# Optimization experiments

Measured on AMD Instinct MI355X. Metric: run time of the kernel, lower is better.

## Reference

```python
import jax, jax.numpy as jnp
import numpy as np

B, N, A, D = 1, 10000, 32, 256
H, DH = 4, 64


def setup_inputs() -> dict:
    key = jax.random.key(0)
    ks = jax.random.split(key, 9)
    x = jax.random.normal(ks[0], (B, N, D), dtype=jnp.float32)
    adj_kv_indices = jax.random.randint(ks[1], (B, N, A), 0, N, dtype=jnp.int64)
    mask = jax.random.randint(ks[2], (B, N, A), 0, 2) > 0
    Wq = jax.random.normal(ks[3], (D, H * DH), dtype=jnp.float32) * 0.02
    Wkv = jax.random.normal(ks[4], (D, 2 * H * DH), dtype=jnp.float32) * 0.02
    Wo = jax.random.normal(ks[5], (H * DH, D), dtype=jnp.float32) * 0.02
    bo = jnp.zeros((D,), dtype=jnp.float32)
    null_k = jax.random.normal(ks[6], (H, DH), dtype=jnp.float32)
    null_v = jax.random.normal(ks[7], (H, DH), dtype=jnp.float32)
    return {"x": x, "adj_kv_indices": adj_kv_indices, "mask": mask,
            "Wq": Wq, "Wkv": Wkv, "Wo": Wo, "bo": bo,
            "null_k": null_k, "null_v": null_v}


def reference(x, adj_kv_indices, mask, Wq, Wkv, Wo, bo, null_k, null_v):
    b, n, d = x.shape
    a = adj_kv_indices.shape[-1]
    h, dh = null_k.shape
    scale = dh ** -0.5

    # gather neighbor features: [b, n, a, d]
    kv_x = jnp.take_along_axis(x, adj_kv_indices.reshape(b, n * a)[:, :, None], axis=1)
    kv_x = kv_x.reshape(b, n, a, d)

    q = (x @ Wq).reshape(b, n, h, dh).transpose(0, 2, 1, 3)          # b h n dh
    kv = kv_x @ Wkv                                                   # b n a 2*h*dh
    k, v = jnp.split(kv, 2, axis=-1)
    k = k.reshape(b, n, a, h, dh).transpose(0, 3, 1, 2, 4)            # b h n a dh
    v = v.reshape(b, n, a, h, dh).transpose(0, 3, 1, 2, 4)

    # prepend null key/value token
    nk = jnp.broadcast_to(null_k[None, :, None, None, :], (b, h, n, 1, dh))
    nv = jnp.broadcast_to(null_v[None, :, None, None, :], (b, h, n, 1, dh))
    k = jnp.concatenate([nk, k], axis=-2)                             # b h n (a+1) dh
    v = jnp.concatenate([nv, v], axis=-2)

    full_mask = jnp.pad(mask, ((0, 0), (0, 0), (1, 0)), constant_values=True)
    full_mask = full_mask[:, None, :, :]                              # b 1 n (a+1)

    sim = jnp.einsum('bhnd,bhnad->bhna', q, k) * scale
    mask_value = -jnp.finfo(sim.dtype).max
    sim = jnp.where(full_mask, sim, mask_value)
    attn = jax.nn.softmax(sim, axis=-1)
    out = jnp.einsum('bhna,bhnad->bhnd', attn, v)
    out = out.transpose(0, 2, 1, 3).reshape(b, n, h * dh)
    return out @ Wo + bo
```

## Files before the change

kernel.cpp:

```cpp
#include <hip/hip_runtime.h>
#include <float.h>


typedef _Float16 f16;
typedef _Float16 f16x4 __attribute__((ext_vector_type(4)));
typedef _Float16 f16x8 __attribute__((ext_vector_type(8)));
typedef float    f32x4 __attribute__((ext_vector_type(4)));

#define BM 64
#define BN 128
#define BK 64
#define LDK 72

__global__ __launch_bounds__(256) void tcast_kernel(
    const float* __restrict__ W, f16* __restrict__ Wt, int K, int Nn, float mul)
{
    __shared__ float s[32][33];
    const int tx = threadIdx.x & 31, ty = threadIdx.x >> 5;
    const int kb = blockIdx.y * 32, nb = blockIdx.x * 32;
#pragma unroll
    for (int r = 0; r < 4; r++)
        s[ty + r * 8][tx] = W[(size_t)(kb + ty + r * 8) * Nn + nb + tx];
    __syncthreads();
#pragma unroll
    for (int r = 0; r < 4; r++)
        Wt[(size_t)(nb + ty + r * 8) * K + kb + tx] = (f16)(s[tx][ty + r * 8] * mul);
}

template <int A_F32, int OUT_HALF>
__global__ __launch_bounds__(256) void hgemm_kernel(
    const void* __restrict__ Av, const f16* __restrict__ Bt,
    void* __restrict__ C, const float* __restrict__ bias,
    int M, int Nn, int K)
{
    __shared__ f16 As[BM][LDK];
    __shared__ f16 Bs[BN][LDK];
    const int tid = threadIdx.x;
    const int w = tid >> 6;
    const int l = tid & 63;
    const int brow = blockIdx.y * BM;
    const int bcol = blockIdx.x * BN;

    const int sra = tid >> 2, sca = (tid & 3) * 16;
    const int srb = tid >> 1, scb = (tid & 1) * 32;
    const int arow = min(brow + sra, M - 1);

    const int fr = l & 15;
    const int k4 = (l >> 4) * 4;

    f32x4 acc[8];
#pragma unroll
    for (int c = 0; c < 8; c++) acc[c] = (f32x4){0.f, 0.f, 0.f, 0.f};

    for (int kk = 0; kk < K; kk += BK) {
        if (A_F32) {
            const float* ap = (const float*)Av + (size_t)arow * K + kk + sca;
#pragma unroll
            for (int i = 0; i < 4; i++) {
                float4 v = ((const float4*)ap)[i];
                f16x4 o = {(f16)v.x, (f16)v.y, (f16)v.z, (f16)v.w};
                *(f16x4*)&As[sra][sca + i * 4] = o;
            }
        } else {
            const f16* ap = (const f16*)Av + (size_t)arow * K + kk + sca;
            *(f16x8*)&As[sra][sca]     = *(const f16x8*)(ap);
            *(f16x8*)&As[sra][sca + 8] = *(const f16x8*)(ap + 8);
        }
        {
            const f16* bp = Bt + (size_t)(bcol + srb) * K + kk + scb;
#pragma unroll
            for (int i = 0; i < 4; i++)
                *(f16x8*)&Bs[srb][scb + i * 8] = *(const f16x8*)(bp + i * 8);
        }
        __syncthreads();
#pragma unroll
        for (int k0 = 0; k0 < BK; k0 += 16) {
            f16x4 af = *(const f16x4*)&As[w * 16 + fr][k0 + k4];
#pragma unroll
            for (int c = 0; c < 8; c++) {
                f16x4 bf = *(const f16x4*)&Bs[c * 16 + fr][k0 + k4];
                acc[c] = __builtin_amdgcn_mfma_f32_16x16x16f16(af, bf, acc[c], 0, 0, 0);
            }
        }
        __syncthreads();
    }

#pragma unroll
    for (int c = 0; c < 8; c++) {
        const int col = bcol + c * 16 + fr;
#pragma unroll
        for (int j = 0; j < 4; j++) {
            const int row = brow + w * 16 + (l >> 4) * 4 + j;
            if (row < M) {
                if (OUT_HALF)
                    ((f16*)C)[(size_t)row * Nn + col] = (f16)acc[c][j];
                else
                    ((float*)C)[(size_t)row * Nn + col] = acc[c][j] + bias[col];
            }
        }
    }
}

__global__ __launch_bounds__(256) void attn_kernel(
    const f16* __restrict__ QKV,
    const int* __restrict__ aidx, const int* __restrict__ amask,
    const float* __restrict__ nullk, const float* __restrict__ nullv,
    f16* __restrict__ out)
{
    const int n    = blockIdx.x;
    const int tid  = threadIdx.x;
    const int w    = tid >> 6;
    const int h    = w;
    const int lane = tid & 63;
    const int g    = lane >> 4;
    const int gl   = lane & 15;

    __shared__ int   sIdx[32];
    __shared__ int   sMsk[32];
    __shared__ float sP[4][33];

    if (tid < 32) {
        sIdx[tid] = aidx[n * 32 + tid];
        sMsk[tid] = amask[n * 32 + tid];
    }
    __syncthreads();

    f16x4 qh = *(const f16x4*)(QKV + (size_t)n * 768 + h * 64 + gl * 4);
    const float q0 = (float)qh[0], q1 = (float)qh[1], q2 = (float)qh[2], q3 = (float)qh[3];

    float sim[9];

    {
        float s;
        if (g == 0) {
            float4 nk4 = ((const float4*)nullk)[h * 16 + gl];
            s = q0 * nk4.x + q1 * nk4.y + q2 * nk4.z + q3 * nk4.w;
        } else {
            int j = sIdx[g - 1];
            f16x4 kh = *(const f16x4*)(QKV + (size_t)j * 768 + 256 + h * 64 + gl * 4);
            s = q0 * (float)kh[0] + q1 * (float)kh[1] + q2 * (float)kh[2] + q3 * (float)kh[3];
        }
        s += __shfl_xor(s, 1); s += __shfl_xor(s, 2);
        s += __shfl_xor(s, 4); s += __shfl_xor(s, 8);
        bool ok = (g == 0) || (sMsk[g - 1] != 0);
        sim[0] = ok ? s : -3.0e38f;
    }

#pragma unroll
    for (int r = 1; r < 9; r++) {
        int a  = r * 4 + g;
        int ai = min(a - 1, 31);
        int j  = sIdx[ai];
        f16x4 kh = *(const f16x4*)(QKV + (size_t)j * 768 + 256 + h * 64 + gl * 4);
        float s = q0 * (float)kh[0] + q1 * (float)kh[1] + q2 * (float)kh[2] + q3 * (float)kh[3];
        s += __shfl_xor(s, 1); s += __shfl_xor(s, 2);
        s += __shfl_xor(s, 4); s += __shfl_xor(s, 8);
        bool ok = (a < 33) && (sMsk[ai] != 0);
        sim[r] = ok ? s : -3.0e38f;
    }

    float m = sim[0];
#pragma unroll
    for (int r = 1; r < 9; r++) m = fmaxf(m, sim[r]);
    m = fmaxf(m, __shfl_xor(m, 16));
    m = fmaxf(m, __shfl_xor(m, 32));

    float p[9]; float l = 0.0f;
#pragma unroll
    for (int r = 0; r < 9; r++) {
        p[r] = (sim[r] > -1.0e37f) ? __expf(sim[r] - m) : 0.0f;
        l += p[r];
    }
    l += __shfl_xor(l, 16);
    l += __shfl_xor(l, 32);
    const float inv = 1.0f / l;

    if (gl == 0) {
#pragma unroll
        for (int r = 0; r < 9; r++) {
            int a = r * 4 + g;
            if (a < 33) sP[w][a] = p[r] * inv;
        }
    }
    __syncthreads();

    float acc = sP[w][0] * nullv[h * 64 + lane];
#pragma unroll
    for (int a = 1; a <= 32; a++) {
        int j = sIdx[a - 1];
        float va = (float)QKV[(size_t)j * 768 + 512 + h * 64 + lane];
        acc += sP[w][a] * va;
    }
    out[(size_t)n * 256 + h * 64 + lane] = (f16)acc;
}

extern "C" void kernel_launch(void* const* d_in, const int* in_sizes, int n_in,
                              void* d_out, int out_size, void* d_ws, size_t ws_size,
                              hipStream_t stream)
{
    const float* x     = (const float*)d_in[0];
    const int*   aidx  = (const int*)  d_in[1];
    const int*   amask = (const int*)  d_in[2];
    const float* Wq    = (const float*)d_in[3];
    const float* Wkv   = (const float*)d_in[4];
    const float* Wo    = (const float*)d_in[5];
    const float* bo    = (const float*)d_in[6];
    const float* nk    = (const float*)d_in[7];
    const float* nv    = (const float*)d_in[8];
    float* out = (float*)d_out;

    const int N = 10000;
    f16* Wqkvt = (f16*)d_ws;
    f16* Wot   = Wqkvt + 768 * 256;
    f16* QKV   = Wot   + 256 * 256;
    f16* AOh   = QKV   + (size_t)N * 768;

    dim3 blk(256);
    tcast_kernel<<<dim3(8,  8), blk, 0, stream>>>(Wq,  Wqkvt,             256, 256, 0.125f);
    tcast_kernel<<<dim3(16, 8), blk, 0, stream>>>(Wkv, Wqkvt + 256 * 256, 256, 512, 1.0f);
    tcast_kernel<<<dim3(8,  8), blk, 0, stream>>>(Wo,  Wot,               256, 256, 1.0f);

    const int gm = (N + BM - 1) / BM;
    hgemm_kernel<1, 1><<<dim3(768 / BN, gm), blk, 0, stream>>>(x,   Wqkvt, QKV, nullptr, N, 768, 256);
    attn_kernel       <<<dim3(N),              blk, 0, stream>>>(QKV, aidx, amask, nk, nv, AOh);
    hgemm_kernel<0, 0><<<dim3(256 / BN, gm), blk, 0, stream>>>(AOh, Wot,   out, bo,      N, 256, 256);
}
```

Baseline: 150.2 us.

## Retile GEMM to 128x128 with direct global-to-LDS loads and 16x16x32 MFMA

The GEMM kernel now uses 128x128 tiles with a 2x2 wave layout. Each wave computes a 64x64 sub-tile as 4x4 MFMA accumulators using the wider 16x16x32 f16 instruction, and tiles are loaded with global_load_lds directly into unpadded LDS. The fp32 x input is no longer converted to f16 inside the GEMM; a separate cast kernel does it beforehand, which adds a launch and an extra round trip of x through memory. The aim is more register-level reuse and fewer LDS store instructions, at the cost of possible LDS bank conflicts from the unpadded layout and fewer blocks for the small output GEMM.

```diff
diff --git a/kernel.cpp b/kernel.cpp
--- a/kernel.cpp
+++ b/kernel.cpp
@@ -1,5 +1,4 @@
 #include <hip/hip_runtime.h>
-#include <float.h>
 
 
 typedef _Float16 f16;
@@ -7,10 +6,29 @@
 typedef _Float16 f16x8 __attribute__((ext_vector_type(8)));
 typedef float    f32x4 __attribute__((ext_vector_type(4)));
 
-#define BM 64
-#define BN 128
-#define BK 64
-#define LDK 72
+#define TM 128
+#define TN 128
+#define TK 32
+
+__device__ __forceinline__ void gload16(const f16* g, f16* l) {
+    __builtin_amdgcn_global_load_lds(
+        (const __attribute__((address_space(1))) unsigned int*)g,
+        (__attribute__((address_space(3))) unsigned int*)l,
+        16, 0, 0);
+}
+
+__global__ __launch_bounds__(256) void cast_kernel(
+    const float* __restrict__ in, f16* __restrict__ out, int n8)
+{
+    int i = blockIdx.x * 256 + threadIdx.x;
+    if (i < n8) {
+        float4 a = ((const float4*)in)[i * 2];
+        float4 b = ((const float4*)in)[i * 2 + 1];
+        f16x8 o = {(f16)a.x, (f16)a.y, (f16)a.z, (f16)a.w,
+                   (f16)b.x, (f16)b.y, (f16)b.z, (f16)b.w};
+        ((f16x8*)out)[i] = o;
+    }
+}
 
 __global__ __launch_bounds__(256) void tcast_kernel(
     const float* __restrict__ W, f16* __restrict__ Wt, int K, int Nn, float mul)
@@ -27,75 +45,69 @@
         Wt[(size_t)(nb + ty + r * 8) * K + kb + tx] = (f16)(s[tx][ty + r * 8] * mul);
 }
 
-template <int A_F32, int OUT_HALF>
+template <int OUT_F32>
 __global__ __launch_bounds__(256) void hgemm_kernel(
-    const void* __restrict__ Av, const f16* __restrict__ Bt,
+    const f16* __restrict__ A, const f16* __restrict__ Bt,
     void* __restrict__ C, const float* __restrict__ bias,
     int M, int Nn, int K)
 {
-    __shared__ f16 As[BM][LDK];
-    __shared__ f16 Bs[BN][LDK];
+    __shared__ f16 As[TM * TK];
+    __shared__ f16 Bs[TN * TK];
     const int tid = threadIdx.x;
-    const int w = tid >> 6;
-    const int l = tid & 63;
-    const int brow = blockIdx.y * BM;
-    const int bcol = blockIdx.x * BN;
-
-    const int sra = tid >> 2, sca = (tid & 3) * 16;
-    const int srb = tid >> 1, scb = (tid & 1) * 32;
-    const int arow = min(brow + sra, M - 1);
-
-    const int fr = l & 15;
-    const int k4 = (l >> 4) * 4;
-
-    f32x4 acc[8];
-#pragma unroll
-    for (int c = 0; c < 8; c++) acc[c] = (f32x4){0.f, 0.f, 0.f, 0.f};
-
-    for (int kk = 0; kk < K; kk += BK) {
-        if (A_F32) {
-            const float* ap = (const float*)Av + (size_t)arow * K + kk + sca;
-#pragma unroll
-            for (int i = 0; i < 4; i++) {
-                float4 v = ((const float4*)ap)[i];
-                f16x4 o = {(f16)v.x, (f16)v.y, (f16)v.z, (f16)v.w};
-                *(f16x4*)&As[sra][sca + i * 4] = o;
-            }
-        } else {
-            const f16* ap = (const f16*)Av + (size_t)arow * K + kk + sca;
-            *(f16x8*)&As[sra][sca]     = *(const f16x8*)(ap);
-            *(f16x8*)&As[sra][sca + 8] = *(const f16x8*)(ap + 8);
-        }
-        {
-            const f16* bp = Bt + (size_t)(bcol + srb) * K + kk + scb;
-#pragma unroll
-            for (int i = 0; i < 4; i++)
-                *(f16x8*)&Bs[srb][scb + i * 8] = *(const f16x8*)(bp + i * 8);
-        }
+    const int w  = tid >> 6, l = tid & 63;
+    const int fr = l & 15,  h = l >> 4;
+    const int brow = blockIdx.y * TM, bcol = blockIdx.x * TN;
+    const int wr = (w >> 1) * 64, wc = (w & 1) * 64;
+
+    const int c1 = tid, c2 = tid + 256;
+    const size_t aoff1 = (size_t)min(brow + (c1 >> 2), M - 1) * K + (c1 & 3) * 8;
+    const size_t aoff2 = (size_t)min(brow + (c2 >> 2), M - 1) * K + (c2 & 3) * 8;
+    const size_t boff1 = (size_t)(bcol + (c1 >> 2)) * K + (c1 & 3) * 8;
+    const size_t boff2 = (size_t)(bcol + (c2 >> 2)) * K + (c2 & 3) * 8;
+
+    f32x4 acc[4][4];
+#pragma unroll
+    for (int m = 0; m < 4; m++)
+#pragma unroll
+        for (int n = 0; n < 4; n++) acc[m][n] = (f32x4){0.f, 0.f, 0.f, 0.f};
+
+    for (int kk = 0; kk < K; kk += TK) {
+        gload16(A  + aoff1 + kk, &As[c1 * 8]);
+        gload16(A  + aoff2 + kk, &As[c2 * 8]);
+        gload16(Bt + boff1 + kk, &Bs[c1 * 8]);
+        gload16(Bt + boff2 + kk, &Bs[c2 * 8]);
         __syncthreads();
-#pragma unroll
-        for (int k0 = 0; k0 < BK; k0 += 16) {
-            f16x4 af = *(const f16x4*)&As[w * 16 + fr][k0 + k4];
-#pragma unroll
-            for (int c = 0; c < 8; c++) {
-                f16x4 bf = *(const f16x4*)&Bs[c * 16 + fr][k0 + k4];
-                acc[c] = __builtin_amdgcn_mfma_f32_16x16x16f16(af, bf, acc[c], 0, 0, 0);
-            }
-        }
+
+        f16x8 af[4], bf[4];
+#pragma unroll
+        for (int m = 0; m < 4; m++)
+            af[m] = *(const f16x8*)&As[(wr + m * 16 + fr) * TK + h * 8];
+#pragma unroll
+        for (int n = 0; n < 4; n++)
+            bf[n] = *(const f16x8*)&Bs[(wc + n * 16 + fr) * TK + h * 8];
+#pragma unroll
+        for (int m = 0; m < 4; m++)
+#pragma unroll
+            for (int n = 0; n < 4; n++)
+                acc[m][n] = __builtin_amdgcn_mfma_f32_16x16x32_f16(
+                    af[m], bf[n], acc[m][n], 0, 0, 0);
         __syncthreads();
     }
 
 #pragma unroll
-    for (int c = 0; c < 8; c++) {
-        const int col = bcol + c * 16 + fr;
-#pragma unroll
-        for (int j = 0; j < 4; j++) {
-            const int row = brow + w * 16 + (l >> 4) * 4 + j;
-            if (row < M) {
-                if (OUT_HALF)
-                    ((f16*)C)[(size_t)row * Nn + col] = (f16)acc[c][j];
-                else
-                    ((float*)C)[(size_t)row * Nn + col] = acc[c][j] + bias[col];
+    for (int m = 0; m < 4; m++) {
+#pragma unroll
+        for (int n = 0; n < 4; n++) {
+            const int col = bcol + wc + n * 16 + fr;
+#pragma unroll
+            for (int j = 0; j < 4; j++) {
+                const int row = brow + wr + m * 16 + h * 4 + j;
+                if (row < M) {
+                    if (OUT_F32)
+                        ((float*)C)[(size_t)row * Nn + col] = acc[m][n][j] + bias[col];
+                    else
+                        ((f16*)C)[(size_t)row * Nn + col] = (f16)acc[m][n][j];
+                }
             }
         }
     }
@@ -210,18 +222,20 @@
     float* out = (float*)d_out;
 
     const int N = 10000;
-    f16* Wqkvt = (f16*)d_ws;
+    f16* xh    = (f16*)d_ws;
+    f16* Wqkvt = xh    + (size_t)N * 256;
     f16* Wot   = Wqkvt + 768 * 256;
     f16* QKV   = Wot   + 256 * 256;
     f16* AOh   = QKV   + (size_t)N * 768;
 
     dim3 blk(256);
+    cast_kernel<<<dim3(N * 256 / 8 / 256 + 1), blk, 0, stream>>>(x, xh, N * 256 / 8);
     tcast_kernel<<<dim3(8,  8), blk, 0, stream>>>(Wq,  Wqkvt,             256, 256, 0.125f);
     tcast_kernel<<<dim3(16, 8), blk, 0, stream>>>(Wkv, Wqkvt + 256 * 256, 256, 512, 1.0f);
     tcast_kernel<<<dim3(8,  8), blk, 0, stream>>>(Wo,  Wot,               256, 256, 1.0f);
 
-    const int gm = (N + BM - 1) / BM;
-    hgemm_kernel<1, 1><<<dim3(768 / BN, gm), blk, 0, stream>>>(x,   Wqkvt, QKV, nullptr, N, 768, 256);
-    attn_kernel       <<<dim3(N),              blk, 0, stream>>>(QKV, aidx, amask, nk, nv, AOh);
-    hgemm_kernel<0, 0><<<dim3(256 / BN, gm), blk, 0, stream>>>(AOh, Wot,   out, bo,      N, 256, 256);
-}
+    const int gm = (N + TM - 1) / TM;
+    hgemm_kernel<0><<<dim3(768 / TN, gm), blk, 0, stream>>>(xh,  Wqkvt, QKV, nullptr, N, 768, 256);
+    attn_kernel    <<<dim3(N),            blk, 0, stream>>>(QKV, aidx, amask, nk, nv, AOh);
+    hgemm_kernel<1><<<dim3(256 / TN, gm), blk, 0, stream>>>(AOh, Wot,   out, bo,      N, 256, 256);
+}
```

New measurement: 153.5 us. 1.02x slower.
